# Performance work log

Hardware: AMD Instinct MI355X
Metric: run time of the kernel (lower is better)

## Reference

```python
import jax, jax.numpy as jnp
import numpy as np
import math

B, S, HID, H = 8, 512, 768, 12
D = HID // H  # 64
LABEL_VOCAB = 2 * 40 + 1  # 81
EPS = 1e-5


def layernorm(x, g, b):
    mu = jnp.mean(x, axis=-1, keepdims=True)
    var = jnp.var(x, axis=-1, keepdims=True)
    return (x - mu) * jax.lax.rsqrt(var + EPS) * g + b


def setup_inputs() -> dict:
    key = jax.random.key(0)
    ks = jax.random.split(key, 12)
    s = 0.02
    return {
        "hidden_states": jax.random.normal(ks[0], (B, S, HID), jnp.float32),
        "attention_mask": jnp.zeros((B, 1, 1, S), jnp.float32),
        "graph_arc": jax.random.randint(ks[1], (B, S, S), 0, LABEL_VOCAB, jnp.int32),
        "Wq": jax.random.normal(ks[2], (HID, HID), jnp.float32) * s,
        "bq": jnp.zeros((HID,), jnp.float32),
        "Wk": jax.random.normal(ks[3], (HID, HID), jnp.float32) * s,
        "bk": jnp.zeros((HID,), jnp.float32),
        "Wv": jax.random.normal(ks[4], (HID, HID), jnp.float32) * s,
        "bv": jnp.zeros((HID,), jnp.float32),
        "rel_k": jax.random.normal(ks[5], (LABEL_VOCAB, D), jnp.float32) * s,
        "rel_v": jax.random.normal(ks[6], (LABEL_VOCAB, D), jnp.float32) * s,
        "ln_k_g": jnp.ones((D,), jnp.float32),
        "ln_k_b": jnp.zeros((D,), jnp.float32),
        "ln_v_g": jnp.ones((D,), jnp.float32),
        "ln_v_b": jnp.zeros((D,), jnp.float32),
    }


def reference(hidden_states, attention_mask, graph_arc, Wq, bq, Wk, bk, Wv, bv,
              rel_k, rel_v, ln_k_g, ln_k_b, ln_v_g, ln_v_b):
    # projections -> [B, H, S, D]
    def split_heads(x):
        return x.reshape(B, S, H, D).transpose(0, 2, 1, 3)

    q = split_heads(hidden_states @ Wq + bq)
    k = split_heads(hidden_states @ Wk + bk)
    v = split_heads(hidden_states @ Wv + bv)

    # relation embeddings [B, S, S, D], layernormed over D
    dp_keys = layernorm(rel_k[graph_arc], ln_k_g, ln_k_b)
    dp_values = layernorm(rel_v[graph_arc], ln_v_g, ln_v_b)

    scores = jnp.einsum('bhqd,bhkd->bhqk', q, k) / math.sqrt(D)
    # relative_matmul_dp: per (b, q-position) GEMM of q[B,S,H,D] with dp_keys^T
    scores = scores + jnp.einsum('bqhd,bqkd->bhqk', q.transpose(0, 2, 1, 3), dp_keys)
    scores = scores + attention_mask

    probs = jax.nn.softmax(scores, axis=-1)  # dropout p=0 (eval)

    ctx = jnp.einsum('bhqk,bhkd->bqhd', probs, v)
    # relative_matmul_dpv
    ctx = ctx + jnp.einsum('bhqk,bqkd->bqhd', probs, dp_values)
    return ctx.reshape(B, S, HID)
```

## Files before the change

### kernel.cpp

```cpp
#include <hip/hip_runtime.h>
#include <hip/hip_bf16.h>

#define BB 8
#define SS 512
#define HIDV 768
#define HH 12
#define DD 64
#define LV 81

typedef __attribute__((ext_vector_type(8))) short short8v;
typedef __attribute__((ext_vector_type(4))) short short4v;
typedef __attribute__((ext_vector_type(4))) float f32x4;

#define MFMA16(a, b, c) __builtin_amdgcn_mfma_f32_16x16x32_bf16(a, b, c, 0, 0, 0)

__device__ __forceinline__ short f2bf(float f) {
    __hip_bfloat16 h = __float2bfloat16(f);
    return *reinterpret_cast<short*>(&h);
}
__device__ __forceinline__ void gload16(const void* g, void* l) {
    __builtin_amdgcn_global_load_lds((const __attribute__((address_space(1))) void*)g,
                                     (__attribute__((address_space(3))) void*)l, 16, 0, 0);
}
__device__ __forceinline__ void ldsAddAsm(float* p, float v) {
    __attribute__((address_space(3))) float* lp =
        (__attribute__((address_space(3))) float*)p;
    asm volatile("ds_add_f32 %0, %1" : : "v"(lp), "v"(v) : "memory");
}

__global__ __launch_bounds__(256) void prep_ln_kernel(
    const float* __restrict__ rel_k, const float* __restrict__ rel_v,
    const float* __restrict__ gk, const float* __restrict__ bk,
    const float* __restrict__ gv, const float* __restrict__ bv,
    short* __restrict__ lnkb, short* __restrict__ lnvT) {
    int t = threadIdx.x;
    if (t < 192) {
        bool isv = (t >= 96);
        int r = isv ? t - 96 : t;
        if (r < LV) {
            const float* row = (isv ? rel_v : rel_k) + r * DD;
            const float* g = isv ? gv : gk;
            const float* be = isv ? bv : bk;
            float mu = 0.f;
            for (int d = 0; d < DD; ++d) mu += row[d];
            mu *= (1.f / DD);
            float var = 0.f;
            for (int d = 0; d < DD; ++d) { float x = row[d] - mu; var += x * x; }
            var *= (1.f / DD);
            float rs = rsqrtf(var + 1e-5f);
            if (!isv) {
                for (int d = 0; d < DD; ++d)
                    lnkb[r * DD + d] = f2bf((row[d] - mu) * rs * g[d] + be[d]);
            } else {
                for (int d = 0; d < DD; ++d)
                    lnvT[d * 96 + r] = f2bf((row[d] - mu) * rs * g[d] + be[d]);
            }
        } else {
            if (!isv) for (int d = 0; d < DD; ++d) lnkb[r * DD + d] = 0;
            else      for (int d = 0; d < DD; ++d) lnvT[d * 96 + r] = 0;
        }
    }
}

#define NCONV 3072
#define NTRANS 1728
#define NARC 64
__global__ __launch_bounds__(256) void prep_fused_kernel(
    const float* __restrict__ hidden, short* __restrict__ hbf,
    const float* __restrict__ Wq, const float* __restrict__ Wk, const float* __restrict__ Wv,
    short* __restrict__ WqT, short* __restrict__ WkT, short* __restrict__ WvT,
    const int* __restrict__ arc, unsigned int* __restrict__ arcP) {
    __shared__ unsigned int sbuf[64 * 129];
    const int bid = blockIdx.x;
    const int tid = threadIdx.x;

    if (bid < NCONV) {
        int i = (bid * 256 + tid) * 4;
        float4 v = *reinterpret_cast<const float4*>(&hidden[i]);
        short4v o; o[0] = f2bf(v.x); o[1] = f2bf(v.y); o[2] = f2bf(v.z); o[3] = f2bf(v.w);
        *reinterpret_cast<short4v*>(&hbf[i]) = o;
    } else if (bid < NCONV + NTRANS) {
        int e = bid - NCONV;
        int z = e / 576, rem = e - z * 576;
        int by = rem / 24, bxx = rem - by * 24;
        const float* W; short* O;
        if (z == 0) { W = Wq; O = WqT; }
        else if (z == 1) { W = Wk; O = WkT; }
        else { W = Wv; O = WvT; }
        float* tile = reinterpret_cast<float*>(sbuf);
        int k0 = by * 32, n0 = bxx * 32;
        int r = tid >> 3, c4 = (tid & 7) * 4;
        float4 v = *reinterpret_cast<const float4*>(&W[(size_t)(k0 + r) * HIDV + n0 + c4]);
        tile[r * 33 + c4 + 0] = v.x; tile[r * 33 + c4 + 1] = v.y;
        tile[r * 33 + c4 + 2] = v.z; tile[r * 33 + c4 + 3] = v.w;
        __syncthreads();
        short4v o;
        o[0] = f2bf(tile[(c4 + 0) * 33 + r]); o[1] = f2bf(tile[(c4 + 1) * 33 + r]);
        o[2] = f2bf(tile[(c4 + 2) * 33 + r]); o[3] = f2bf(tile[(c4 + 3) * 33 + r]);
        *reinterpret_cast<short4v*>(&O[(size_t)(n0 + r) * HIDV + k0 + c4]) = o;
    } else {
        int e = bid - NCONV - NTRANS;
        int b = e >> 3, q0 = (e & 7) * 64;
        unsigned int* tbuf = sbuf;
        for (int i = tid; i < 64 * 128; i += 256) {
            int r = i >> 7, c4 = i & 127;
            int4 v = *reinterpret_cast<const int4*>(
                &arc[((size_t)(b * SS) + q0 + r) * SS + 4 * c4]);
            tbuf[r * 129 + c4] = (unsigned)(v.x & 255) | ((unsigned)(v.y & 255) << 8) |
                                 ((unsigned)(v.z & 255) << 16) | ((unsigned)(v.w & 255) << 24);
        }
        __syncthreads();
        for (int i = tid; i < 128 * 64; i += 256) {
            int k4 = i >> 6, r = i & 63;
            arcP[((size_t)b * 128 + k4) * SS + q0 + r] = tbuf[r * 129 + k4];
        }
    }
}

__global__ __launch_bounds__(256) void qkv_gemm_kernel(
    const short* __restrict__ Abf,
    const short* __restrict__ WqT, const short* __restrict__ WkT, const short* __restrict__ WvT,
    const float* __restrict__ bq, const float* __restrict__ bk, const float* __restrict__ bv,
    short* __restrict__ qo, short* __restrict__ ko, short* __restrict__ vto) {
    const short* Bt; const float* bias;
    int z = blockIdx.z;
    if (z == 0) { Bt = WqT; bias = bq; }
    else if (z == 1) { Bt = WkT; bias = bk; }
    else { Bt = WvT; bias = bv; }

    __shared__ short smem[8192];
    short* As = smem;
    short* Bs = smem + 4096;

    const int tid = threadIdx.x;
    const int lane = tid & 63, w = tid >> 6;
    const int li = lane & 15, g = lane >> 4;
    const int wr = w >> 1, wc = w & 1;
    const int m0 = blockIdx.y * 64, n0 = blockIdx.x * 64;

    f32x4 acc[2][2];
    for (int ra = 0; ra < 2; ++ra)
        for (int cb = 0; cb < 2; ++cb)
            for (int r = 0; r < 4; ++r) acc[ra][cb][r] = 0.f;

#pragma unroll 1
    for (int k0 = 0; k0 < HIDV; k0 += 64) {
#pragma unroll
        for (int j = 0; j < 2; ++j) {
            int c = j * 256 + tid;
            int row = c >> 3, s = c & 7;
            int src = s ^ (row & 7);
            gload16(Abf + (size_t)(m0 + row) * HIDV + k0 + src * 8, As + c * 8);
            gload16(Bt + (size_t)(n0 + row) * HIDV + k0 + src * 8, Bs + c * 8);
        }
        __syncthreads();
#pragma unroll
        for (int c = 0; c < 2; ++c) {
            short8v af[2], bf[2];
#pragma unroll
            for (int ra = 0; ra < 2; ++ra) {
                int row = 32 * wr + 16 * ra + li;
                int chunk = (4 * c + g) ^ (row & 7);
                af[ra] = *reinterpret_cast<const short8v*>(&As[row * 64 + chunk * 8]);
            }
#pragma unroll
            for (int cb = 0; cb < 2; ++cb) {
                int rowb = 32 * wc + 16 * cb + li;
                int chunk = (4 * c + g) ^ (rowb & 7);
                bf[cb] = *reinterpret_cast<const short8v*>(&Bs[rowb * 64 + chunk * 8]);
            }
#pragma unroll
            for (int ra = 0; ra < 2; ++ra)
#pragma unroll
                for (int cb = 0; cb < 2; ++cb)
                    acc[ra][cb] = MFMA16(af[ra], bf[cb], acc[ra][cb]);
        }
        __syncthreads();
    }

    const int h = n0 >> 6;
    const int bidx = m0 >> 9;
    if (z < 2) {
        short* dst = (z == 0) ? qo : ko;
        float sc = (z == 0) ? 1.f : 0.125f;
#pragma unroll
        for (int ra = 0; ra < 2; ++ra)
#pragma unroll
            for (int cb = 0; cb < 2; ++cb) {
                int n = 32 * wc + 16 * cb + li;
                float bv_ = bias[n0 + n];
#pragma unroll
                for (int r = 0; r < 4; ++r) {
                    int m = m0 + 32 * wr + 16 * ra + 4 * g + r;
                    int s = m & 511;
                    dst[(((size_t)bidx * HH + h) * SS + s) * DD + n] =
                        f2bf((acc[ra][cb][r] + bv_) * sc);
                }
            }
    } else {
        short* Cs = smem;
#pragma unroll
        for (int ra = 0; ra < 2; ++ra)
#pragma unroll
            for (int cb = 0; cb < 2; ++cb) {
                int nl = 32 * wc + 16 * cb + li;
                float bv_ = bias[n0 + nl];
#pragma unroll
                for (int r = 0; r < 4; ++r) {
                    int ml = 32 * wr + 16 * ra + 4 * g + r;
                    Cs[nl * 72 + ml] = f2bf(acc[ra][cb][r] + bv_);
                }
            }
        __syncthreads();
        for (int c = tid; c < 512; c += 256) {
            int dl = c >> 3, s8 = (c & 7) * 8;
            short8v vv = *reinterpret_cast<const short8v*>(&Cs[dl * 72 + s8]);
            *reinterpret_cast<short8v*>(
                &vto[(((size_t)bidx * HH + h) * DD + dl) * SS + (m0 & 511) + s8]) = vv;
        }
    }
}

__global__ __launch_bounds__(256, 2) void attn_kernel(
    const short* __restrict__ qb, const short* __restrict__ kb, const short* __restrict__ vt,
    const unsigned int* __restrict__ arcP, const float* __restrict__ maskp,
    const short* __restrict__ lnkb, const short* __restrict__ lnvT,
    float* __restrict__ outp) {
    __shared__ float qlds[4][16][84];
    __shared__ float bucket[4][16][100];

    const int tid = threadIdx.x;
    const int w = tid >> 6, lane = tid & 63;
    const int li = lane & 15, g = lane >> 4;
    const int bx = blockIdx.x;
    const int b = bx & 7;
    const int rest = bx >> 3;
    const int h = rest % HH, qt = rest / HH;
    const int bh = b * HH + h;
    const int q0 = qt * 64 + w * 16;

    const short* kbp = kb + (size_t)bh * SS * DD;
    const short* vbp = vt + (size_t)bh * DD * SS;
    const unsigned int* apb = arcP + (size_t)b * 128 * SS;
    const float* mkb = maskp + (size_t)b * SS;

    for (int i = lane; i < 16 * 100; i += 64) (&bucket[w][0][0])[i] = 0.f;

    short8v qf0, qf1;
    {
        const short* qrow = qb + ((size_t)bh * SS + q0 + li) * DD + 8 * g;
        qf0 = *reinterpret_cast<const short8v*>(qrow);
        qf1 = *reinterpret_cast<const short8v*>(qrow + 32);
    }

#pragma unroll
    for (int ct = 0; ct < 6; ++ct) {
        f32x4 a = {0.f, 0.f, 0.f, 0.f};
        short8v b0 = *reinterpret_cast<const short8v*>(&lnkb[(16 * ct + li) * DD + 8 * g]);
        short8v b1 = *reinterpret_cast<const short8v*>(&lnkb[(16 * ct + li) * DD + 32 + 8 * g]);
        a = MFMA16(qf0, b0, a);
        a = MFMA16(qf1, b1, a);
        if (16 * ct + li < 84)
#pragma unroll
            for (int r = 0; r < 4; ++r) qlds[w][4 * g + r][16 * ct + li] = a[r];
    }

    f32x4 oacc[4];
    for (int t = 0; t < 4; ++t) for (int r = 0; r < 4; ++r) oacc[t][r] = 0.f;

    short8v kf[8];
    short4v vreg[16];
    unsigned int a_[2][4];
    float4 m_[2][4];
    float qv_[2][16];
#pragma unroll
    for (int t = 0; t < 4; ++t) {
        const short* kr = kbp + (size_t)(16 * t + li) * DD + 8 * g;
        kf[2 * t] = *reinterpret_cast<const short8v*>(kr);
        kf[2 * t + 1] = *reinterpret_cast<const short8v*>(kr + 32);
        a_[0][t] = apb[(size_t)(4 * t + g) * SS + q0 + li];
        m_[0][t] = *reinterpret_cast<const float4*>(&mkb[16 * t + 4 * g]);
    }
#pragma unroll
    for (int t = 0; t < 4; ++t) {
        const unsigned int a4 = a_[0][t];
        qv_[0][4 * t + 0] = qlds[w][li][a4 & 255];
        qv_[0][4 * t + 1] = qlds[w][li][(a4 >> 8) & 255];
        qv_[0][4 * t + 2] = qlds[w][li][(a4 >> 16) & 255];
        qv_[0][4 * t + 3] = qlds[w][li][a4 >> 24];
    }

#pragma unroll
    for (int kt = 0; kt < 8; ++kt) {
        const int cur = kt & 1, nxt = cur ^ 1;
        const int kb0 = kt * 64;

        f32x4 sacc[4];
#pragma unroll
        for (int t = 0; t < 4; ++t) {
            f32x4 a = {0.f, 0.f, 0.f, 0.f};
            a = MFMA16(kf[2 * t], qf0, a);
            a = MFMA16(kf[2 * t + 1], qf1, a);
            sacc[t] = a;
        }

#pragma unroll
        for (int dt = 0; dt < 2; ++dt)
#pragma unroll
            for (int t2 = 0; t2 < 4; ++t2) {
                const short* vr = vbp + (size_t)(16 * t2 + li) * SS + kb0 + 32 * dt + 4 * g;
                vreg[8 * dt + 2 * t2 + 0] = *reinterpret_cast<const short4v*>(vr);
                vreg[8 * dt + 2 * t2 + 1] = *reinterpret_cast<const short4v*>(vr + 16);
            }
        if (kt < 7) {
#pragma unroll
            for (int t = 0; t < 4; ++t) {
                const short* kr = kbp + (size_t)(kb0 + 64 + 16 * t + li) * DD + 8 * g;
                kf[2 * t] = *reinterpret_cast<const short8v*>(kr);
                kf[2 * t + 1] = *reinterpret_cast<const short8v*>(kr + 32);
                a_[nxt][t] = apb[(size_t)((kt + 1) * 16 + 4 * t + g) * SS + q0 + li];
                m_[nxt][t] = *reinterpret_cast<const float4*>(&mkb[kb0 + 64 + 16 * t + 4 * g]);
            }
#pragma unroll
            for (int t = 0; t < 4; ++t) {
                const unsigned int a4 = a_[nxt][t];
                qv_[nxt][4 * t + 0] = qlds[w][li][a4 & 255];
                qv_[nxt][4 * t + 1] = qlds[w][li][(a4 >> 8) & 255];
                qv_[nxt][4 * t + 2] = qlds[w][li][(a4 >> 16) & 255];
                qv_[nxt][4 * t + 3] = qlds[w][li][a4 >> 24];
            }
        }

        float p[16];
#pragma unroll
        for (int t = 0; t < 4; ++t) {
            p[4 * t + 0] = __expf(sacc[t][0] + qv_[cur][4 * t + 0] + m_[cur][t].x);
            p[4 * t + 1] = __expf(sacc[t][1] + qv_[cur][4 * t + 1] + m_[cur][t].y);
            p[4 * t + 2] = __expf(sacc[t][2] + qv_[cur][4 * t + 2] + m_[cur][t].z);
            p[4 * t + 3] = __expf(sacc[t][3] + qv_[cur][4 * t + 3] + m_[cur][t].w);
        }

#pragma unroll
        for (int t = 0; t < 4; ++t) {
            const unsigned int a4 = a_[cur][t];
            ldsAddAsm(&bucket[w][li][a4 & 255], p[4 * t + 0]);
            ldsAddAsm(&bucket[w][li][(a4 >> 8) & 255], p[4 * t + 1]);
            ldsAddAsm(&bucket[w][li][(a4 >> 16) & 255], p[4 * t + 2]);
            ldsAddAsm(&bucket[w][li][a4 >> 24], p[4 * t + 3]);
        }

        short8v pfrag[2];
#pragma unroll
        for (int t = 0; t < 4; ++t)
#pragma unroll
            for (int r = 0; r < 4; ++r) pfrag[t >> 1][4 * (t & 1) + r] = f2bf(p[4 * t + r]);
#pragma unroll
        for (int dt = 0; dt < 2; ++dt) {
#pragma unroll
            for (int t2 = 0; t2 < 4; ++t2) {
                short4v v0 = vreg[8 * dt + 2 * t2 + 0];
                short4v v1 = vreg[8 * dt + 2 * t2 + 1];
                short8v vf;
                vf[0] = v0[0]; vf[1] = v0[1]; vf[2] = v0[2]; vf[3] = v0[3];
                vf[4] = v1[0]; vf[5] = v1[1]; vf[6] = v1[2]; vf[7] = v1[3];
                oacc[t2] = MFMA16(pfrag[dt], vf, oacc[t2]);
            }
        }
    }

    float lsum = 0.f;
#pragma unroll
    for (int j = 0; j < 24; ++j) {
        int c = 24 * g + j;
        lsum += (c < 81) ? bucket[w][li][c] : 0.f;
    }
    lsum += __shfl_xor(lsum, 16);
    lsum += __shfl_xor(lsum, 32);
    float inv = 1.f / lsum;
    float invr[4];
#pragma unroll
    for (int r = 0; r < 4; ++r) invr[r] = __shfl(inv, 4 * g + r);

    f32x4 racc[4];
    for (int t = 0; t < 4; ++t) for (int r = 0; r < 4; ++r) racc[t][r] = 0.f;
#pragma unroll
    for (int c = 0; c < 3; ++c) {
        f32x4 b0 = *reinterpret_cast<const f32x4*>(&bucket[w][li][8 * g + 32 * c]);
        f32x4 b1 = *reinterpret_cast<const f32x4*>(&bucket[w][li][8 * g + 32 * c + 4]);
        short8v bfr;
        bfr[0] = f2bf(b0[0]); bfr[1] = f2bf(b0[1]); bfr[2] = f2bf(b0[2]); bfr[3] = f2bf(b0[3]);
        bfr[4] = f2bf(b1[0]); bfr[5] = f2bf(b1[1]); bfr[6] = f2bf(b1[2]); bfr[7] = f2bf(b1[3]);
#pragma unroll
        for (int t2 = 0; t2 < 4; ++t2) {
            short8v lf = *reinterpret_cast<const short8v*>(
                &lnvT[(16 * t2 + li) * 96 + 8 * g + 32 * c]);
            racc[t2] = MFMA16(bfr, lf, racc[t2]);
        }
    }

#pragma unroll
    for (int t2 = 0; t2 < 4; ++t2)
#pragma unroll
        for (int r = 0; r < 4; ++r) {
            int row = q0 + 4 * g + r;
            outp[((size_t)b * SS + row) * HIDV + h * DD + 16 * t2 + li] =
                (oacc[t2][r] + racc[t2][r]) * invr[r];
        }
}

extern "C" void kernel_launch(void* const* d_in, const int* in_sizes, int n_in,
                              void* d_out, int out_size, void* d_ws, size_t ws_size,
                              hipStream_t stream) {
    const float* hidden = (const float*)d_in[0];
    const float* mask   = (const float*)d_in[1];
    const int*   arc    = (const int*)d_in[2];
    const float* Wq = (const float*)d_in[3];
    const float* bq = (const float*)d_in[4];
    const float* Wk = (const float*)d_in[5];
    const float* bk = (const float*)d_in[6];
    const float* Wv = (const float*)d_in[7];
    const float* bv = (const float*)d_in[8];
    const float* rel_k = (const float*)d_in[9];
    const float* rel_v = (const float*)d_in[10];
    const float* lng_k = (const float*)d_in[11];
    const float* lnb_k = (const float*)d_in[12];
    const float* lng_v = (const float*)d_in[13];
    const float* lnb_v = (const float*)d_in[14];
    float* out = (float*)d_out;

    char* p = (char*)d_ws;
    auto carve = [&](size_t bytes) { char* r = p; p += (bytes + 255) & ~(size_t)255; return r; };
    short* lnkb = (short*)carve((size_t)96 * DD * 2);
    short* lnvT = (short*)carve((size_t)DD * 96 * 2);
    short* hbf  = (short*)carve((size_t)BB * SS * HIDV * 2);
    short* WqT  = (short*)carve((size_t)HIDV * HIDV * 2);
    short* WkT  = (short*)carve((size_t)HIDV * HIDV * 2);
    short* WvT  = (short*)carve((size_t)HIDV * HIDV * 2);
    const size_t per = (size_t)BB * HH * SS * DD;
    short* qbuf = (short*)carve(per * 2);
    short* kbuf = (short*)carve(per * 2);
    short* vtb  = (short*)carve(per * 2);
    unsigned int* arcP = (unsigned int*)carve((size_t)BB * 128 * SS * 4);

    prep_ln_kernel<<<1, 256, 0, stream>>>(rel_k, rel_v, lng_k, lnb_k, lng_v, lnb_v, lnkb, lnvT);
    prep_fused_kernel<<<dim3(NCONV + NTRANS + NARC), 256, 0, stream>>>(
        hidden, hbf, Wq, Wk, Wv, WqT, WkT, WvT, arc, arcP);
    qkv_gemm_kernel<<<dim3(HIDV / 64, (BB * SS) / 64, 3), 256, 0, stream>>>(
        hbf, WqT, WkT, WvT, bq, bk, bv, qbuf, kbuf, vtb);
    attn_kernel<<<dim3(BB * HH * 8), 256, 0, stream>>>(
        qbuf, kbuf, vtb, arcP, mask, lnkb, lnvT, out);
}
```

Baseline: 191.9 us.

## Split attention key range across two blocks and add combine kernel

The attention kernel is split along the key dimension into two halves, doubling the grid from 768 to 1536 blocks. Each half writes its unnormalized output accumulators and label-bucket probability sums to a workspace buffer. A new combine kernel adds the two partials, forms the row sum, applies the relative-value GEMM and normalizes. This targets low occupancy, since 768 blocks give only a few waves on the GPU. In exchange it adds an extra launch and a global round-trip of partial results. It relies on the softmax having no max subtraction, so the two halves can be summed directly.

```diff
diff --git a/kernel.cpp b/kernel.cpp
--- a/kernel.cpp
+++ b/kernel.cpp
@@ -7,6 +7,7 @@
 #define HH 12
 #define DD 64
 #define LV 81
+#define PART_STRIDE 10240
 
 typedef __attribute__((ext_vector_type(8))) short short8v;
 typedef __attribute__((ext_vector_type(4))) short short4v;
@@ -221,11 +222,10 @@
     }
 }
 
-__global__ __launch_bounds__(256, 2) void attn_kernel(
+__global__ __launch_bounds__(256, 2) void attn_half_kernel(
     const short* __restrict__ qb, const short* __restrict__ kb, const short* __restrict__ vt,
     const unsigned int* __restrict__ arcP, const float* __restrict__ maskp,
-    const short* __restrict__ lnkb, const short* __restrict__ lnvT,
-    float* __restrict__ outp) {
+    const short* __restrict__ lnkb, float* __restrict__ part) {
     __shared__ float qlds[4][16][84];
     __shared__ float bucket[4][16][100];
 
@@ -233,16 +233,20 @@
     const int w = tid >> 6, lane = tid & 63;
     const int li = lane & 15, g = lane >> 4;
     const int bx = blockIdx.x;
-    const int b = bx & 7;
-    const int rest = bx >> 3;
+    const int half = bx & 1;
+    const int bxx = bx >> 1;
+    const int b = bxx & 7;
+    const int rest = bxx >> 3;
     const int h = rest % HH, qt = rest / HH;
     const int bh = b * HH + h;
     const int q0 = qt * 64 + w * 16;
+    const int kt0 = half * 4;
 
     const short* kbp = kb + (size_t)bh * SS * DD;
     const short* vbp = vt + (size_t)bh * DD * SS;
     const unsigned int* apb = arcP + (size_t)b * 128 * SS;
     const float* mkb = maskp + (size_t)b * SS;
+    float* pbase = part + ((size_t)(bh * 8 + qt) * 2 + half) * PART_STRIDE;
 
     for (int i = lane; i < 16 * 100; i += 64) (&bucket[w][0][0])[i] = 0.f;
 
@@ -275,11 +279,11 @@
     float qv_[2][16];
 #pragma unroll
     for (int t = 0; t < 4; ++t) {
-        const short* kr = kbp + (size_t)(16 * t + li) * DD + 8 * g;
+        const short* kr = kbp + (size_t)(kt0 * 64 + 16 * t + li) * DD + 8 * g;
         kf[2 * t] = *reinterpret_cast<const short8v*>(kr);
         kf[2 * t + 1] = *reinterpret_cast<const short8v*>(kr + 32);
-        a_[0][t] = apb[(size_t)(4 * t + g) * SS + q0 + li];
-        m_[0][t] = *reinterpret_cast<const float4*>(&mkb[16 * t + 4 * g]);
+        a_[0][t] = apb[(size_t)(kt0 * 16 + 4 * t + g) * SS + q0 + li];
+        m_[0][t] = *reinterpret_cast<const float4*>(&mkb[kt0 * 64 + 16 * t + 4 * g]);
     }
 #pragma unroll
     for (int t = 0; t < 4; ++t) {
@@ -291,9 +295,9 @@
     }
 
 #pragma unroll
-    for (int kt = 0; kt < 8; ++kt) {
-        const int cur = kt & 1, nxt = cur ^ 1;
-        const int kb0 = kt * 64;
+    for (int ktL = 0; ktL < 4; ++ktL) {
+        const int cur = ktL & 1, nxt = cur ^ 1;
+        const int kb0 = (kt0 + ktL) * 64;
 
         f32x4 sacc[4];
 #pragma unroll
@@ -312,13 +316,13 @@
                 vreg[8 * dt + 2 * t2 + 0] = *reinterpret_cast<const short4v*>(vr);
                 vreg[8 * dt + 2 * t2 + 1] = *reinterpret_cast<const short4v*>(vr + 16);
             }
-        if (kt < 7) {
+        if (ktL < 3) {
 #pragma unroll
             for (int t = 0; t < 4; ++t) {
                 const short* kr = kbp + (size_t)(kb0 + 64 + 16 * t + li) * DD + 8 * g;
                 kf[2 * t] = *reinterpret_cast<const short8v*>(kr);
                 kf[2 * t + 1] = *reinterpret_cast<const short8v*>(kr + 32);
-                a_[nxt][t] = apb[(size_t)((kt + 1) * 16 + 4 * t + g) * SS + q0 + li];
+                a_[nxt][t] = apb[(size_t)((kt0 + ktL + 1) * 16 + 4 * t + g) * SS + q0 + li];
                 m_[nxt][t] = *reinterpret_cast<const float4*>(&mkb[kb0 + 64 + 16 * t + 4 * g]);
             }
 #pragma unroll
@@ -368,11 +372,52 @@
         }
     }
 
+    float* po = pbase;
+    float* pb = pbase + 4096;
+#pragma unroll
+    for (int t2 = 0; t2 < 4; ++t2)
+#pragma unroll
+        for (int r = 0; r < 4; ++r)
+            po[(size_t)(w * 16 + 4 * g + r) * 64 + 16 * t2 + li] = oacc[t2][r];
+    for (int i = lane; i < 16 * 96; i += 64)
+        pb[(size_t)(w * 16 + i / 96) * 96 + (i % 96)] = bucket[w][i / 96][i % 96];
+}
+
+__global__ __launch_bounds__(256, 2) void combine_kernel(
+    const float* __restrict__ part, const short* __restrict__ lnvT,
+    float* __restrict__ outp) {
+    __shared__ float tbl[4][16][96];
+
+    const int tid = threadIdx.x;
+    const int w = tid >> 6, lane = tid & 63;
+    const int li = lane & 15, g = lane >> 4;
+    const int bx = blockIdx.x;
+    const int bh = bx >> 3, qt = bx & 7;
+    const int b = bh / HH, h = bh % HH;
+    const int q0 = qt * 64;
+
+    const float* pA = part + ((size_t)(bh * 8 + qt) * 2 + 0) * PART_STRIDE;
+    const float* pB = part + ((size_t)(bh * 8 + qt) * 2 + 1) * PART_STRIDE;
+
+    for (int i = lane; i < 16 * 96; i += 64) {
+        size_t off = 4096 + (size_t)(w * 16 + i / 96) * 96 + (i % 96);
+        tbl[w][i / 96][i % 96] = pA[off] + pB[off];
+    }
+
+    f32x4 oacc[4];
+#pragma unroll
+    for (int t2 = 0; t2 < 4; ++t2)
+#pragma unroll
+        for (int r = 0; r < 4; ++r) {
+            size_t off = (size_t)(w * 16 + 4 * g + r) * 64 + 16 * t2 + li;
+            oacc[t2][r] = pA[off] + pB[off];
+        }
+
     float lsum = 0.f;
 #pragma unroll
     for (int j = 0; j < 24; ++j) {
         int c = 24 * g + j;
-        lsum += (c < 81) ? bucket[w][li][c] : 0.f;
+        lsum += (c < 81) ? tbl[w][li][c] : 0.f;
     }
     lsum += __shfl_xor(lsum, 16);
     lsum += __shfl_xor(lsum, 32);
@@ -385,8 +430,8 @@
     for (int t = 0; t < 4; ++t) for (int r = 0; r < 4; ++r) racc[t][r] = 0.f;
 #pragma unroll
     for (int c = 0; c < 3; ++c) {
-        f32x4 b0 = *reinterpret_cast<const f32x4*>(&bucket[w][li][8 * g + 32 * c]);
-        f32x4 b1 = *reinterpret_cast<const f32x4*>(&bucket[w][li][8 * g + 32 * c + 4]);
+        f32x4 b0 = *reinterpret_cast<const f32x4*>(&tbl[w][li][8 * g + 32 * c]);
+        f32x4 b1 = *reinterpret_cast<const f32x4*>(&tbl[w][li][8 * g + 32 * c + 4]);
         short8v bfr;
         bfr[0] = f2bf(b0[0]); bfr[1] = f2bf(b0[1]); bfr[2] = f2bf(b0[2]); bfr[3] = f2bf(b0[3]);
         bfr[4] = f2bf(b1[0]); bfr[5] = f2bf(b1[1]); bfr[6] = f2bf(b1[2]); bfr[7] = f2bf(b1[3]);
@@ -402,7 +447,7 @@
     for (int t2 = 0; t2 < 4; ++t2)
 #pragma unroll
         for (int r = 0; r < 4; ++r) {
-            int row = q0 + 4 * g + r;
+            int row = q0 + w * 16 + 4 * g + r;
             outp[((size_t)b * SS + row) * HIDV + h * DD + 16 * t2 + li] =
                 (oacc[t2][r] + racc[t2][r]) * invr[r];
         }
@@ -441,12 +486,14 @@
     short* kbuf = (short*)carve(per * 2);
     short* vtb  = (short*)carve(per * 2);
     unsigned int* arcP = (unsigned int*)carve((size_t)BB * 128 * SS * 4);
+    float* partials = (float*)carve((size_t)BB * HH * 8 * 2 * PART_STRIDE * 4);
 
     prep_ln_kernel<<<1, 256, 0, stream>>>(rel_k, rel_v, lng_k, lnb_k, lng_v, lnb_v, lnkb, lnvT);
     prep_fused_kernel<<<dim3(NCONV + NTRANS + NARC), 256, 0, stream>>>(
         hidden, hbf, Wq, Wk, Wv, WqT, WkT, WvT, arc, arcP);
     qkv_gemm_kernel<<<dim3(HIDV / 64, (BB * SS) / 64, 3), 256, 0, stream>>>(
         hbf, WqT, WkT, WvT, bq, bk, bv, qbuf, kbuf, vtb);
-    attn_kernel<<<dim3(BB * HH * 8), 256, 0, stream>>>(
-        qbuf, kbuf, vtb, arcP, mask, lnkb, lnvT, out);
-}
+    attn_half_kernel<<<dim3(BB * HH * 8 * 2), 256, 0, stream>>>(
+        qbuf, kbuf, vtb, arcP, mask, lnkb, partials);
+    combine_kernel<<<dim3(BB * HH * 8), 256, 0, stream>>>(partials, lnvT, out);
+}
```

New measurement: 211.7 us. 10.3% more time.
